# Performance work log

Hardware: AMD Instinct MI355X
Metric: run time of the kernel (lower is better)

The kernel has to match this reference:

```python
import jax, jax.numpy as jnp
import numpy as np

H = W = 56
WS = 7            # window size
SHIFT = 3
HEADS = 6
DIM = 192
N = WS * WS       # tokens per window (49)
NW = (H // WS) * (W // WS)  # windows per image (64)
EPS = 1e-5


def _rel_pos_index():
    coords = np.stack(np.meshgrid(np.arange(WS), np.arange(WS), indexing='ij'))
    cf = coords.reshape(2, -1)
    rel = (cf[:, :, None] - cf[:, None, :]).transpose(1, 2, 0)
    rel[:, :, 0] += WS - 1
    rel[:, :, 1] += WS - 1
    rel[:, :, 0] *= 2 * WS - 1
    return rel.sum(-1).astype(np.int32)  # [N, N]


def _attn_mask():
    img = np.zeros([1, H, W, 1], dtype=np.float32)
    slices = (slice(0, -WS), slice(-WS, -SHIFT), slice(-SHIFT, None))
    cnt = 0
    for hs in slices:
        for ws_ in slices:
            img[:, hs, ws_, :] = cnt
            cnt += 1
    m = img.reshape(1, H // WS, WS, W // WS, WS, 1).transpose(0, 1, 3, 2, 4, 5)
    m = m.reshape(-1, N)                      # [nW, N]
    diff = m[:, None, :] - m[:, :, None]
    return np.where(diff != 0, -100.0, 0.0).astype(np.float32)  # [nW, N, N]

_RPI = _rel_pos_index()
_MASK = _attn_mask()


def _ln(x, g, b):
    mu = jnp.mean(x, axis=-1, keepdims=True)
    var = jnp.mean(jnp.square(x - mu), axis=-1, keepdims=True)
    return (x - mu) * jax.lax.rsqrt(var + EPS) * g + b


def setup_inputs() -> dict:
    key = jax.random.key(0)
    ks = jax.random.split(key, 12)
    C, Hd = DIM, DIM * 4
    s = lambda n: 1.0 / np.sqrt(n)
    return {
        'x': jax.random.normal(ks[0], (32, H * W, C), jnp.float32),
        'norm1_g': jnp.ones((C,), jnp.float32),
        'norm1_b': jnp.zeros((C,), jnp.float32),
        'qkv_w': jax.random.normal(ks[1], (C, 3 * C), jnp.float32) * s(C),
        'qkv_b': jnp.zeros((3 * C,), jnp.float32),
        'bias_table': jax.random.normal(ks[2], ((2 * WS - 1) ** 2, HEADS), jnp.float32) * 0.02,
        'proj_w': jax.random.normal(ks[3], (C, C), jnp.float32) * s(C),
        'proj_b': jnp.zeros((C,), jnp.float32),
        'norm2_g': jnp.ones((C,), jnp.float32),
        'norm2_b': jnp.zeros((C,), jnp.float32),
        'fc1_w': jax.random.normal(ks[4], (C, Hd), jnp.float32) * s(C),
        'fc1_b': jnp.zeros((Hd,), jnp.float32),
        'fc2_w': jax.random.normal(ks[5], (Hd, C), jnp.float32) * s(Hd),
        'fc2_b': jnp.zeros((C,), jnp.float32),
    }


def reference(x, norm1_g, norm1_b, qkv_w, qkv_b, bias_table, proj_w, proj_b,
              norm2_g, norm2_b, fc1_w, fc1_b, fc2_w, fc2_b):
    B, L, C = x.shape
    hd = C // HEADS
    scale = hd ** -0.5

    shortcut = x
    h = _ln(x, norm1_g, norm1_b).reshape(B, H, W, C)
    h = jnp.roll(h, (-SHIFT, -SHIFT), axis=(1, 2))

    # window partition -> [B*nW, N, C]
    h = h.reshape(B, H // WS, WS, W // WS, WS, C).transpose(0, 1, 3, 2, 4, 5)
    xw = h.reshape(B * NW, N, C)

    qkv = (xw @ qkv_w + qkv_b).reshape(B * NW, N, 3, HEADS, hd)
    q, k, v = jnp.moveaxis(qkv, 2, 0)                 # each [B*nW, N, H, d]
    q = jnp.swapaxes(q, 1, 2) * scale                 # [B*nW, H, N, d]
    k = jnp.swapaxes(k, 1, 2)
    v = jnp.swapaxes(v, 1, 2)

    attn = jnp.einsum('whnd,whmd->whnm', q, k)        # [B*nW, H, N, N]
    bias = bias_table[jnp.asarray(_RPI).reshape(-1)].reshape(N, N, HEADS)
    attn = attn + jnp.transpose(bias, (2, 0, 1))[None]
    mask = jnp.asarray(_MASK)                         # [nW, N, N]
    attn = attn.reshape(B, NW, HEADS, N, N) + mask[None, :, None]
    attn = jax.nn.softmax(attn.reshape(B * NW, HEADS, N, N), axis=-1)

    out = jnp.einsum('whnm,whmd->whnd', attn, v)      # [B*nW, H, N, d]
    out = jnp.swapaxes(out, 1, 2).reshape(B * NW, N, C)
    out = out @ proj_w + proj_b

    # window reverse -> [B, H, W, C]
    out = out.reshape(B, H // WS, W // WS, WS, WS, C).transpose(0, 1, 3, 2, 4, 5)
    out = out.reshape(B, H, W, C)
    out = jnp.roll(out, (SHIFT, SHIFT), axis=(1, 2)).reshape(B, L, C)

    x = shortcut + out
    hmlp = _ln(x, norm2_g, norm2_b)
    hmlp = jax.nn.gelu(hmlp @ fc1_w + fc1_b, approximate=False) @ fc2_w + fc2_b
    return x + hmlp
```

## Files before the change

### kernel.cpp

```cpp
#include <hip/hip_runtime.h>
#include <hip/hip_bf16.h>
#include <math.h>

static constexpr int CB     = 32;
static constexpr int CH     = 56;
static constexpr int CW     = 56;
static constexpr int CC     = 192;
static constexpr int CSHIFT = 3;
static constexpr int CN     = 49;
static constexpr int CNW    = 64;
static constexpr int CL     = CH * CW;
static constexpr int CM     = CB * CNW * CN;
static constexpr int CHID   = 768;

typedef __attribute__((ext_vector_type(8))) __bf16 bf16x8;
typedef __attribute__((ext_vector_type(4))) float  f32x4;

__device__ __forceinline__ float bfu2f(unsigned short u) {
  union { unsigned i; float f; } c; c.i = (unsigned)u << 16; return c.f;
}
__device__ __forceinline__ unsigned short f2bu(float f) {
  __hip_bfloat16 b = __float2bfloat16(f);
  return *(unsigned short*)&b;
}
__device__ __forceinline__ float gelu_fast(float v) {
  float e = __expf(-1.702f * v);
  return __fdividef(v, 1.0f + e);
}

#define GLOAD16(g, l) __builtin_amdgcn_global_load_lds( \
    (__attribute__((address_space(1))) void*)(g),       \
    (__attribute__((address_space(3))) void*)(l), 16, 0, 0)

__global__ __launch_bounds__(256)
void prep_kernel(const float* __restrict__ qkv_w, const float* __restrict__ proj_w,
                 const float* __restrict__ fc1_w, const float* __restrict__ fc2_w,
                 const float* __restrict__ btab,
                 __hip_bfloat16* __restrict__ wq, __hip_bfloat16* __restrict__ wp,
                 __hip_bfloat16* __restrict__ w1, __hip_bfloat16* __restrict__ w2,
                 float* __restrict__ bias2)
{
  int idx = blockIdx.x * 256 + threadIdx.x;
  if (idx < 110592) {
    int k = idx / 576, n = idx - k * 576;
    wq[n * 192 + k] = __float2bfloat16(qkv_w[idx]);
    return;
  }
  idx -= 110592;
  if (idx < 36864) {
    int k = idx / 192, n = idx - k * 192;
    wp[n * 192 + k] = __float2bfloat16(proj_w[idx]);
    return;
  }
  idx -= 36864;
  if (idx < 147456) {
    int k = idx / 768, n = idx - k * 768;
    w1[n * 192 + k] = __float2bfloat16(fc1_w[idx]);
    return;
  }
  idx -= 147456;
  if (idx < 147456) {
    int k = idx / 192, n = idx - k * 192;
    w2[n * 768 + k] = __float2bfloat16(fc2_w[idx]);
    return;
  }
  idx -= 147456;
  if (idx < 98304) {
    int j = idx & 63, i = (idx >> 6) & 63;
    int rest = idx >> 12;
    int h = rest % 6, wt = rest / 6;
    float val;
    if (i >= 49 || j >= 49) {
      val = -INFINITY;
    } else {
      int ti = i / 7, ci = i - ti * 7;
      int tj = j / 7, cj = j - tj * 7;
      val = btab[((ti - tj + 6) * 13 + (ci - cj + 6)) * 6 + h];
      int hri = (wt & 2) ? ((ti < 4) ? 1 : 2) : 0;
      int hci = (wt & 1) ? ((ci < 4) ? 1 : 2) : 0;
      int hrj = (wt & 2) ? ((tj < 4) ? 1 : 2) : 0;
      int hcj = (wt & 1) ? ((cj < 4) ? 1 : 2) : 0;
      if (hri * 3 + hci != hrj * 3 + hcj) val -= 100.0f;
    }
    bias2[idx] = val;
  }
}

template<bool ROLL>
__global__ __launch_bounds__(256)
void ln_kernel(const float* __restrict__ xin, const float* __restrict__ gamma,
               const float* __restrict__ beta, __hip_bfloat16* __restrict__ out)
{
  const int wid = threadIdx.x >> 6, lane = threadIdx.x & 63;
  const int m = blockIdx.x * 4 + wid;
  size_t src;
  if (ROLL) {
    int b   = m / (CNW * CN);
    int rem = m - b * (CNW * CN);
    int nw  = rem / CN, t = rem - nw * CN;
    int wr = nw >> 3, wc = nw & 7;
    int ti = t / 7, tj = t - ti * 7;
    int sr = wr * 7 + ti + CSHIFT; if (sr >= CH) sr -= CH;
    int sc = wc * 7 + tj + CSHIFT; if (sc >= CW) sc -= CW;
    src = ((size_t)b * CL + (size_t)sr * CW + sc) * CC;
  } else {
    src = (size_t)m * CC;
  }
  float v0 = xin[src + lane], v1 = xin[src + lane + 64], v2 = xin[src + lane + 128];
  float s  = v0 + v1 + v2;
  float sq = v0 * v0 + v1 * v1 + v2 * v2;
  #pragma unroll
  for (int off = 32; off; off >>= 1) { s += __shfl_xor(s, off); sq += __shfl_xor(sq, off); }
  const float mu  = s * (1.0f / CC);
  const float inv = rsqrtf(sq * (1.0f / CC) - mu * mu + 1e-5f);
  const size_t dst = (size_t)m * CC;
  out[dst + lane      ] = __float2bfloat16((v0 - mu) * inv * gamma[lane      ] + beta[lane      ]);
  out[dst + lane + 64 ] = __float2bfloat16((v1 - mu) * inv * gamma[lane + 64 ] + beta[lane + 64 ]);
  out[dst + lane + 128] = __float2bfloat16((v2 - mu) * inv * gamma[lane + 128] + beta[lane + 128]);
}

template<int K, int N, int BN, int MODE>
__global__ __launch_bounds__(256)
void gemm_mfma(const __hip_bfloat16* __restrict__ Ain, const __hip_bfloat16* __restrict__ Wt,
               const float* __restrict__ bias, void* __restrict__ Outv,
               const float* __restrict__ resid)
{
  constexpr int NT = BN / 32;
  __shared__ short As[128 * 64];
  __shared__ short Bs[BN * 64];

  const int tid  = threadIdx.x;
  const int lane = tid & 63, wid = tid >> 6;

  const int nbx = N / BN;
  const int nwg = nbx * gridDim.y;
  const int wg  = blockIdx.y * nbx + blockIdx.x;
  const int swz = (wg & 7) * (nwg >> 3) + (wg >> 3);
  const int row0 = (swz / nbx) * 128, col0 = (swz % nbx) * BN;

  const int wm = wid >> 1, wn = wid & 1;
  const int lr = lane & 15, lg = lane >> 4;

  const short* A  = (const short*)Ain;
  const short* W  = (const short*)Wt;

  f32x4 acc[4][NT] = {};

  #pragma unroll
  for (int kk = 0; kk < K; kk += 64) {
    #pragma unroll
    for (int it = 0; it < 4; ++it) {
      int c = it * 256 + tid;
      int row = c >> 3, slot = c & 7;
      int kg = (slot ^ (row & 7)) * 8;
      GLOAD16(A + (size_t)(row0 + row) * K + kk + kg, As + c * 8);
    }
    #pragma unroll
    for (int it = 0; it < BN / 32; ++it) {
      int c = it * 256 + tid;
      int row = c >> 3, slot = c & 7;
      int kg = (slot ^ (row & 7)) * 8;
      GLOAD16(W + (size_t)(col0 + row) * K + kk + kg, Bs + c * 8);
    }
    __syncthreads();

    #pragma unroll
    for (int kh = 0; kh < 2; ++kh) {
      const int sb = kh * 4 + lg;
      bf16x8 bfr[NT];
      #pragma unroll
      for (int nt = 0; nt < NT; ++nt) {
        int br = wn * (BN / 2) + nt * 16 + lr;
        bfr[nt] = *(const bf16x8*)(Bs + br * 64 + (sb ^ (br & 7)) * 8);
      }
      #pragma unroll
      for (int m = 0; m < 4; ++m) {
        int ar = wm * 64 + m * 16 + lr;
        bf16x8 afr = *(const bf16x8*)(As + ar * 64 + (sb ^ (ar & 7)) * 8);
        #pragma unroll
        for (int nt = 0; nt < NT; ++nt)
          acc[m][nt] = __builtin_amdgcn_mfma_f32_16x16x32_bf16(afr, bfr[nt], acc[m][nt], 0, 0, 0);
      }
    }
    __syncthreads();
  }

  const int colA = col0 + wn * (BN / 2) + lr;
  float bv[NT];
  #pragma unroll
  for (int nt = 0; nt < NT; ++nt) bv[nt] = bias[colA + nt * 16];

  #pragma unroll
  for (int m = 0; m < 4; ++m) {
    #pragma unroll
    for (int r = 0; r < 4; ++r) {
      const int mrow = row0 + wm * 64 + m * 16 + lg * 4 + r;
      if (MODE == 0) {
        __hip_bfloat16* O = (__hip_bfloat16*)Outv;
        const size_t rr = (size_t)mrow * N + colA;
        #pragma unroll
        for (int nt = 0; nt < NT; ++nt)
          O[rr + nt * 16] = __float2bfloat16(acc[m][nt][r] + bv[nt]);
      } else if (MODE == 1) {
        int b = mrow / (CNW * CN);
        int rem = mrow - b * (CNW * CN);
        int nw = rem / CN, t = rem - nw * CN;
        int wr = nw >> 3, wc = nw & 7;
        int ti = t / 7, tj = t - ti * 7;
        int dr = wr * 7 + ti + CSHIFT; if (dr >= CH) dr -= CH;
        int dc = wc * 7 + tj + CSHIFT; if (dc >= CW) dc -= CW;
        const size_t dst = ((size_t)b * CL + (size_t)dr * CW + dc) * CC + colA;
        float* O = (float*)Outv;
        #pragma unroll
        for (int nt = 0; nt < NT; ++nt)
          O[dst + nt * 16] = resid[dst + nt * 16] + acc[m][nt][r] + bv[nt];
      } else if (MODE == 2) {
        __hip_bfloat16* O = (__hip_bfloat16*)Outv;
        const size_t rr = (size_t)mrow * N + colA;
        #pragma unroll
        for (int nt = 0; nt < NT; ++nt)
          O[rr + nt * 16] = __float2bfloat16(gelu_fast(acc[m][nt][r] + bv[nt]));
      } else {
        float* O = (float*)Outv;
        const size_t rr = (size_t)mrow * N + colA;
        #pragma unroll
        for (int nt = 0; nt < NT; ++nt)
          O[rr + nt * 16] = resid[rr + nt * 16] + acc[m][nt][r] + bv[nt];
      }
    }
  }
}

__global__ __launch_bounds__(64)
void attn_mfma_kernel(const __hip_bfloat16* __restrict__ qkv,
                      const float* __restrict__ bias2,
                      __hip_bfloat16* __restrict__ attnout)
{
  __shared__ unsigned short VT[32 * 72];
  __shared__ unsigned short Pl[64 * 72];

  const int bid = blockIdx.x;
  const int w = bid / 6, h = bid - (bid / 6) * 6;
  const int lane = threadIdx.x;
  const int lr = lane & 15, lg = lane >> 4;
  const int nw = w & 63;
  const int wt = (((nw >> 3) == 7) ? 2 : 0) + (((nw & 7) == 7) ? 1 : 0);
  const unsigned short* Q = (const unsigned short*)qkv;
  const size_t rowbase = (size_t)w * 49 * 576;
  const float scale = 0.17677669529663687f;

  for (int e = lane; e < 196; e += 64) {
    int t = e % 49, c = e / 49;
    uint4 v = *(const uint4*)(Q + rowbase + (size_t)t * 576 + 384 + h * 32 + c * 8);
    unsigned va[4] = {v.x, v.y, v.z, v.w};
    #pragma unroll
    for (int q = 0; q < 4; ++q) {
      VT[(c * 8 + q * 2    ) * 72 + t] = (unsigned short)(va[q] & 0xffff);
      VT[(c * 8 + q * 2 + 1) * 72 + t] = (unsigned short)(va[q] >> 16);
    }
  }
  for (int e = lane; e < 32 * 15; e += 64) {
    int d = e / 15, t = 49 + e - (e / 15) * 15;
    VT[d * 72 + t] = 0;
  }

  bf16x8 qf[4], kf[4];
  #pragma unroll
  for (int it = 0; it < 4; ++it) {
    int tok = it * 16 + lr; if (tok > 48) tok = 48;
    qf[it] = *(const bf16x8*)(Q + rowbase + (size_t)tok * 576 + h * 32 + lg * 8);
  }
  #pragma unroll
  for (int jt = 0; jt < 4; ++jt) {
    int tok = jt * 16 + lr; if (tok > 48) tok = 48;
    kf[jt] = *(const bf16x8*)(Q + rowbase + (size_t)tok * 576 + 192 + h * 32 + lg * 8);
  }

  f32x4 acc[4][4] = {};
  __builtin_amdgcn_s_setprio(1);
  #pragma unroll
  for (int jt = 0; jt < 4; ++jt)
    #pragma unroll
    for (int it = 0; it < 4; ++it)
      acc[jt][it] = __builtin_amdgcn_mfma_f32_16x16x32_bf16(kf[jt], qf[it], acc[jt][it], 0, 0, 0);
  __builtin_amdgcn_s_setprio(0);

  __syncthreads();

  const float* brow = bias2 + ((size_t)(wt * 6 + h) * 64) * 64;
  #pragma unroll
  for (int it = 0; it < 4; ++it) {
    const int i = it * 16 + lr;
    float s[4][4];
    #pragma unroll
    for (int jt = 0; jt < 4; ++jt) {
      float4 bv = *(const float4*)(brow + (size_t)i * 64 + jt * 16 + lg * 4);
      s[jt][0] = fmaf(acc[jt][it][0], scale, bv.x);
      s[jt][1] = fmaf(acc[jt][it][1], scale, bv.y);
      s[jt][2] = fmaf(acc[jt][it][2], scale, bv.z);
      s[jt][3] = fmaf(acc[jt][it][3], scale, bv.w);
    }
    float mx = s[0][0];
    #pragma unroll
    for (int jt = 0; jt < 4; ++jt)
      #pragma unroll
      for (int r = 0; r < 4; ++r) mx = fmaxf(mx, s[jt][r]);
    mx = fmaxf(mx, __shfl_xor(mx, 16));
    mx = fmaxf(mx, __shfl_xor(mx, 32));
    float sum = 0.0f;
    #pragma unroll
    for (int jt = 0; jt < 4; ++jt)
      #pragma unroll
      for (int r = 0; r < 4; ++r) { s[jt][r] = __expf(s[jt][r] - mx); sum += s[jt][r]; }
    sum += __shfl_xor(sum, 16);
    sum += __shfl_xor(sum, 32);
    const float inv = 1.0f / sum;
    #pragma unroll
    for (int jt = 0; jt < 4; ++jt) {
      unsigned lo = (unsigned)f2bu(s[jt][0] * inv) | ((unsigned)f2bu(s[jt][1] * inv) << 16);
      unsigned hi = (unsigned)f2bu(s[jt][2] * inv) | ((unsigned)f2bu(s[jt][3] * inv) << 16);
      uint2 val; val.x = lo; val.y = hi;
      *(uint2*)&Pl[i * 72 + jt * 16 + lg * 4] = val;
    }
  }

  __syncthreads();

  f32x4 o[4][2] = {};
  #pragma unroll
  for (int ks = 0; ks < 2; ++ks) {
    bf16x8 pa[4], vb[2];
    #pragma unroll
    for (int it = 0; it < 4; ++it)
      pa[it] = *(const bf16x8*)&Pl[(it * 16 + lr) * 72 + ks * 32 + lg * 8];
    #pragma unroll
    for (int nt = 0; nt < 2; ++nt)
      vb[nt] = *(const bf16x8*)&VT[(nt * 16 + lr) * 72 + ks * 32 + lg * 8];
    __builtin_amdgcn_s_setprio(1);
    #pragma unroll
    for (int it = 0; it < 4; ++it) {
      o[it][0] = __builtin_amdgcn_mfma_f32_16x16x32_bf16(pa[it], vb[0], o[it][0], 0, 0, 0);
      o[it][1] = __builtin_amdgcn_mfma_f32_16x16x32_bf16(pa[it], vb[1], o[it][1], 0, 0, 0);
    }
    __builtin_amdgcn_s_setprio(0);
  }

  #pragma unroll
  for (int it = 0; it < 4; ++it) {
    #pragma unroll
    for (int r = 0; r < 4; ++r) {
      int i = it * 16 + lg * 4 + r;
      if (i < 49) {
        size_t dst = ((size_t)w * 49 + i) * 192 + h * 32;
        attnout[dst + lr]      = __float2bfloat16(o[it][0][r]);
        attnout[dst + 16 + lr] = __float2bfloat16(o[it][1][r]);
      }
    }
  }
}

extern "C" void kernel_launch(void* const* d_in, const int* in_sizes, int n_in,
                              void* d_out, int out_size, void* d_ws, size_t ws_size,
                              hipStream_t stream)
{
  const float* x        = (const float*)d_in[0];
  const float* n1g      = (const float*)d_in[1];
  const float* n1b      = (const float*)d_in[2];
  const float* qkv_w    = (const float*)d_in[3];
  const float* qkv_b    = (const float*)d_in[4];
  const float* btab     = (const float*)d_in[5];
  const float* proj_w   = (const float*)d_in[6];
  const float* proj_b   = (const float*)d_in[7];
  const float* n2g      = (const float*)d_in[8];
  const float* n2b      = (const float*)d_in[9];
  const float* fc1_w    = (const float*)d_in[10];
  const float* fc1_b    = (const float*)d_in[11];
  const float* fc2_w    = (const float*)d_in[12];
  const float* fc2_b    = (const float*)d_in[13];
  float* out = (float*)d_out;

  char* ws = (char*)d_ws;
  const size_t szA = (size_t)CM * CC * 2;
  const size_t szB = (size_t)CM * CHID * 2;
  __hip_bfloat16* bufA = (__hip_bfloat16*)ws;
  __hip_bfloat16* bufB = (__hip_bfloat16*)(ws + szA);
  __hip_bfloat16* wq   = (__hip_bfloat16*)(ws + szA + szB);
  __hip_bfloat16* wp   = wq + 576 * 192;
  __hip_bfloat16* w1   = wp + 192 * 192;
  __hip_bfloat16* w2   = w1 + 768 * 192;
  float* bias2         = (float*)(w2 + 192 * 768);

  const int prep_total = 110592 + 36864 + 147456 + 147456 + 98304;
  prep_kernel<<<(prep_total + 255) / 256, 256, 0, stream>>>(
      qkv_w, proj_w, fc1_w, fc2_w, btab, wq, wp, w1, w2, bias2);

  ln_kernel<true><<<CM / 4, 256, 0, stream>>>(x, n1g, n1b, bufA);
  gemm_mfma<192, 576, 96, 0><<<dim3(576 / 96, CM / 128), 256, 0, stream>>>(bufA, wq, qkv_b, bufB, nullptr);
  attn_mfma_kernel<<<2048 * 6, 64, 0, stream>>>(bufB, bias2, bufA);
  gemm_mfma<192, 192, 64, 1><<<dim3(192 / 64, CM / 128), 256, 0, stream>>>(bufA, wp, proj_b, out, x);
  ln_kernel<false><<<CM / 4, 256, 0, stream>>>(out, n2g, n2b, bufA);
  gemm_mfma<192, CHID, 128, 2><<<dim3(CHID / 128, CM / 128), 256, 0, stream>>>(bufA, w1, fc1_b, bufB, nullptr);
  gemm_mfma<CHID, 192, 64, 3><<<dim3(192 / 64, CM / 128), 256, 0, stream>>>(bufB, w2, fc2_b, out, out);
}
```

Measured before the change: 336.8 us.

## Store residual trunk in bf16 and pass attention probabilities through registers

When the workspace is large enough, the post-attention residual is written to a bf16 buffer rather than fp32. That buffer is read by LayerNorm 2 and as the residual in the fc2 epilogue, cutting the bytes moved for the intermediate trunk. In the attention kernel, the softmax probabilities are no longer staged in LDS behind a barrier. They are rearranged across lanes with shuffles straight into MFMA operand layout, and V fragments are preloaded. The bf16 trunk loses precision in the residual path, and the extra shuffles add ALU work.

```diff
diff --git a/kernel.cpp b/kernel.cpp
--- a/kernel.cpp
+++ b/kernel.cpp
@@ -86,9 +86,9 @@
   }
 }
 
-template<bool ROLL>
+template<bool ROLL, bool BIN>
 __global__ __launch_bounds__(256)
-void ln_kernel(const float* __restrict__ xin, const float* __restrict__ gamma,
+void ln_kernel(const void* __restrict__ xin, const float* __restrict__ gamma,
                const float* __restrict__ beta, __hip_bfloat16* __restrict__ out)
 {
   const int wid = threadIdx.x >> 6, lane = threadIdx.x & 63;
@@ -106,7 +106,11 @@
   } else {
     src = (size_t)m * CC;
   }
-  float v0 = xin[src + lane], v1 = xin[src + lane + 64], v2 = xin[src + lane + 128];
+  const float* xf = (const float*)xin;
+  const unsigned short* xb = (const unsigned short*)xin;
+  float v0 = BIN ? bfu2f(xb[src + lane      ]) : xf[src + lane      ];
+  float v1 = BIN ? bfu2f(xb[src + lane + 64 ]) : xf[src + lane + 64 ];
+  float v2 = BIN ? bfu2f(xb[src + lane + 128]) : xf[src + lane + 128];
   float s  = v0 + v1 + v2;
   float sq = v0 * v0 + v1 * v1 + v2 * v2;
   #pragma unroll
@@ -123,7 +127,7 @@
 __global__ __launch_bounds__(256)
 void gemm_mfma(const __hip_bfloat16* __restrict__ Ain, const __hip_bfloat16* __restrict__ Wt,
                const float* __restrict__ bias, void* __restrict__ Outv,
-               const float* __restrict__ resid)
+               const void* __restrict__ residv)
 {
   constexpr int NT = BN / 32;
   __shared__ short As[128 * 64];
@@ -201,7 +205,7 @@
         #pragma unroll
         for (int nt = 0; nt < NT; ++nt)
           O[rr + nt * 16] = __float2bfloat16(acc[m][nt][r] + bv[nt]);
-      } else if (MODE == 1) {
+      } else if (MODE == 1 || MODE == 4) {
         int b = mrow / (CNW * CN);
         int rem = mrow - b * (CNW * CN);
         int nw = rem / CN, t = rem - nw * CN;
@@ -210,22 +214,38 @@
         int dr = wr * 7 + ti + CSHIFT; if (dr >= CH) dr -= CH;
         int dc = wc * 7 + tj + CSHIFT; if (dc >= CW) dc -= CW;
         const size_t dst = ((size_t)b * CL + (size_t)dr * CW + dc) * CC + colA;
-        float* O = (float*)Outv;
-        #pragma unroll
-        for (int nt = 0; nt < NT; ++nt)
-          O[dst + nt * 16] = resid[dst + nt * 16] + acc[m][nt][r] + bv[nt];
+        const float* resid = (const float*)residv;
+        if (MODE == 1) {
+          float* O = (float*)Outv;
+          #pragma unroll
+          for (int nt = 0; nt < NT; ++nt)
+            O[dst + nt * 16] = resid[dst + nt * 16] + acc[m][nt][r] + bv[nt];
+        } else {
+          __hip_bfloat16* O = (__hip_bfloat16*)Outv;
+          #pragma unroll
+          for (int nt = 0; nt < NT; ++nt)
+            O[dst + nt * 16] = __float2bfloat16(resid[dst + nt * 16] + acc[m][nt][r] + bv[nt]);
+        }
       } else if (MODE == 2) {
         __hip_bfloat16* O = (__hip_bfloat16*)Outv;
         const size_t rr = (size_t)mrow * N + colA;
         #pragma unroll
         for (int nt = 0; nt < NT; ++nt)
           O[rr + nt * 16] = __float2bfloat16(gelu_fast(acc[m][nt][r] + bv[nt]));
-      } else {
+      } else if (MODE == 3) {
         float* O = (float*)Outv;
+        const float* resid = (const float*)residv;
         const size_t rr = (size_t)mrow * N + colA;
         #pragma unroll
         for (int nt = 0; nt < NT; ++nt)
           O[rr + nt * 16] = resid[rr + nt * 16] + acc[m][nt][r] + bv[nt];
+      } else {
+        float* O = (float*)Outv;
+        const unsigned short* resid = (const unsigned short*)residv;
+        const size_t rr = (size_t)mrow * N + colA;
+        #pragma unroll
+        for (int nt = 0; nt < NT; ++nt)
+          O[rr + nt * 16] = bfu2f(resid[rr + nt * 16]) + acc[m][nt][r] + bv[nt];
       }
     }
   }
@@ -237,7 +257,6 @@
                       __hip_bfloat16* __restrict__ attnout)
 {
   __shared__ unsigned short VT[32 * 72];
-  __shared__ unsigned short Pl[64 * 72];
 
   const int bid = blockIdx.x;
   const int w = bid / 6, h = bid - (bid / 6) * 6;
@@ -287,7 +306,17 @@
 
   __syncthreads();
 
+  bf16x8 vb[2][2];
+  #pragma unroll
+  for (int ks = 0; ks < 2; ++ks)
+    #pragma unroll
+    for (int nt = 0; nt < 2; ++nt)
+      vb[ks][nt] = *(const bf16x8*)&VT[(nt * 16 + lr) * 72 + ks * 32 + lg * 8];
+
   const float* brow = bias2 + ((size_t)(wt * 6 + h) * 64) * 64;
+  const int src0 = lr + ((lg & 1) << 5);
+  f32x4 o[4][2] = {};
+
   #pragma unroll
   for (int it = 0; it < 4; ++it) {
     const int i = it * 16 + lr;
@@ -315,34 +344,28 @@
     sum += __shfl_xor(sum, 16);
     sum += __shfl_xor(sum, 32);
     const float inv = 1.0f / sum;
+
+    unsigned wpk[4][2];
     #pragma unroll
     for (int jt = 0; jt < 4; ++jt) {
-      unsigned lo = (unsigned)f2bu(s[jt][0] * inv) | ((unsigned)f2bu(s[jt][1] * inv) << 16);
-      unsigned hi = (unsigned)f2bu(s[jt][2] * inv) | ((unsigned)f2bu(s[jt][3] * inv) << 16);
-      uint2 val; val.x = lo; val.y = hi;
-      *(uint2*)&Pl[i * 72 + jt * 16 + lg * 4] = val;
-    }
-  }
-
-  __syncthreads();
-
-  f32x4 o[4][2] = {};
-  #pragma unroll
-  for (int ks = 0; ks < 2; ++ks) {
-    bf16x8 pa[4], vb[2];
-    #pragma unroll
-    for (int it = 0; it < 4; ++it)
-      pa[it] = *(const bf16x8*)&Pl[(it * 16 + lr) * 72 + ks * 32 + lg * 8];
-    #pragma unroll
-    for (int nt = 0; nt < 2; ++nt)
-      vb[nt] = *(const bf16x8*)&VT[(nt * 16 + lr) * 72 + ks * 32 + lg * 8];
-    __builtin_amdgcn_s_setprio(1);
-    #pragma unroll
-    for (int it = 0; it < 4; ++it) {
-      o[it][0] = __builtin_amdgcn_mfma_f32_16x16x32_bf16(pa[it], vb[0], o[it][0], 0, 0, 0);
-      o[it][1] = __builtin_amdgcn_mfma_f32_16x16x32_bf16(pa[it], vb[1], o[it][1], 0, 0, 0);
-    }
-    __builtin_amdgcn_s_setprio(0);
+      wpk[jt][0] = (unsigned)f2bu(s[jt][0] * inv) | ((unsigned)f2bu(s[jt][1] * inv) << 16);
+      wpk[jt][1] = (unsigned)f2bu(s[jt][2] * inv) | ((unsigned)f2bu(s[jt][3] * inv) << 16);
+    }
+    #pragma unroll
+    for (int ks = 0; ks < 2; ++ks) {
+      union { bf16x8 v; unsigned u[4]; } pa;
+      #pragma unroll
+      for (int wd = 0; wd < 4; ++wd) {
+        const int src = src0 + ((wd >> 1) << 4);
+        unsigned v0 = (unsigned)__shfl((int)wpk[ks * 2    ][wd & 1], src);
+        unsigned v1 = (unsigned)__shfl((int)wpk[ks * 2 + 1][wd & 1], src);
+        pa.u[wd] = (lg & 2) ? v1 : v0;
+      }
+      __builtin_amdgcn_s_setprio(1);
+      o[it][0] = __builtin_amdgcn_mfma_f32_16x16x32_bf16(pa.v, vb[ks][0], o[it][0], 0, 0, 0);
+      o[it][1] = __builtin_amdgcn_mfma_f32_16x16x32_bf16(pa.v, vb[ks][1], o[it][1], 0, 0, 0);
+      __builtin_amdgcn_s_setprio(0);
+    }
   }
 
   #pragma unroll
@@ -382,6 +405,8 @@
   char* ws = (char*)d_ws;
   const size_t szA = (size_t)CM * CC * 2;
   const size_t szB = (size_t)CM * CHID * 2;
+  const size_t szW = (size_t)(110592 + 36864 + 147456 + 147456) * 2;
+  const size_t szb2 = (size_t)98304 * 4;
   __hip_bfloat16* bufA = (__hip_bfloat16*)ws;
   __hip_bfloat16* bufB = (__hip_bfloat16*)(ws + szA);
   __hip_bfloat16* wq   = (__hip_bfloat16*)(ws + szA + szB);
@@ -389,16 +414,27 @@
   __hip_bfloat16* w1   = wp + 192 * 192;
   __hip_bfloat16* w2   = w1 + 768 * 192;
   float* bias2         = (float*)(w2 + 192 * 768);
+  __hip_bfloat16* bufC = (__hip_bfloat16*)(ws + szA + szB + szW + szb2);
+
+  const bool bf16trunk = ws_size >= szA + szB + szW + szb2 + szA;
 
   const int prep_total = 110592 + 36864 + 147456 + 147456 + 98304;
   prep_kernel<<<(prep_total + 255) / 256, 256, 0, stream>>>(
       qkv_w, proj_w, fc1_w, fc2_w, btab, wq, wp, w1, w2, bias2);
 
-  ln_kernel<true><<<CM / 4, 256, 0, stream>>>(x, n1g, n1b, bufA);
+  ln_kernel<true, false><<<CM / 4, 256, 0, stream>>>(x, n1g, n1b, bufA);
   gemm_mfma<192, 576, 96, 0><<<dim3(576 / 96, CM / 128), 256, 0, stream>>>(bufA, wq, qkv_b, bufB, nullptr);
   attn_mfma_kernel<<<2048 * 6, 64, 0, stream>>>(bufB, bias2, bufA);
-  gemm_mfma<192, 192, 64, 1><<<dim3(192 / 64, CM / 128), 256, 0, stream>>>(bufA, wp, proj_b, out, x);
-  ln_kernel<false><<<CM / 4, 256, 0, stream>>>(out, n2g, n2b, bufA);
-  gemm_mfma<192, CHID, 128, 2><<<dim3(CHID / 128, CM / 128), 256, 0, stream>>>(bufA, w1, fc1_b, bufB, nullptr);
-  gemm_mfma<CHID, 192, 64, 3><<<dim3(192 / 64, CM / 128), 256, 0, stream>>>(bufB, w2, fc2_b, out, out);
-}
+
+  if (bf16trunk) {
+    gemm_mfma<192, 192, 64, 4><<<dim3(192 / 64, CM / 128), 256, 0, stream>>>(bufA, wp, proj_b, bufC, x);
+    ln_kernel<false, true><<<CM / 4, 256, 0, stream>>>(bufC, n2g, n2b, bufA);
+    gemm_mfma<192, CHID, 128, 2><<<dim3(CHID / 128, CM / 128), 256, 0, stream>>>(bufA, w1, fc1_b, bufB, nullptr);
+    gemm_mfma<CHID, 192, 64, 5><<<dim3(192 / 64, CM / 128), 256, 0, stream>>>(bufB, w2, fc2_b, out, bufC);
+  } else {
+    gemm_mfma<192, 192, 64, 1><<<dim3(192 / 64, CM / 128), 256, 0, stream>>>(bufA, wp, proj_b, out, x);
+    ln_kernel<false, false><<<CM / 4, 256, 0, stream>>>(out, n2g, n2b, bufA);
+    gemm_mfma<192, CHID, 128, 2><<<dim3(CHID / 128, CM / 128), 256, 0, stream>>>(bufA, w1, fc1_b, bufB, nullptr);
+    gemm_mfma<CHID, 192, 64, 3><<<dim3(192 / 64, CM / 128), 256, 0, stream>>>(bufB, w2, fc2_b, out, out);
+  }
+}
```

New measurement: 316.7 us. 1.06x faster.
